# Kernel optimization log

Hardware: AMD Instinct MI355X
Metric: run time of the kernel (lower is better)

The kernel has to match this reference:

```python
import jax, jax.numpy as jnp
import numpy as np

# Circuit structure constants (HCLT-style tensorized probabilistic circuit)
V = 128      # num_vars
M = 256      # num_latents (input nodes per variable)
C = 64       # num categories per variable
B = 256      # batch size
L = 4        # number of inner (prod, sum) layer pairs
N = 32768    # sum nodes per inner layer
K = 4        # sum-node fanin (children product elements per sum node)
A = 2        # product-node arity
E = N * K    # product elements per layer
NUM_INPUT = V * M


def setup_inputs() -> dict:
    key = jax.random.key(0)
    k1, k2, k3, k4 = jax.random.split(key, 4)
    inputs = jax.random.randint(k1, (B, V), 0, C)                          # [B, V] categorical data
    input_logits = jax.random.normal(k2, (NUM_INPUT, C), dtype=jnp.float32)  # per input-node categorical logits
    sum_logits = jax.random.normal(k3, (L, N, K), dtype=jnp.float32)         # per sum-node edge logits (grouped softmax)
    root_logits = jax.random.normal(k4, (N,), dtype=jnp.float32)             # root sum-node edge logits
    # Irregular child index structure: prod element e in layer l gathers A children
    # from any node computed so far (dummy node 0 excluded, indices >= 1).
    rng = np.random.default_rng(0)
    base = 1 + NUM_INPUT
    child = np.stack([rng.integers(1, base + l * N, size=(E, A)) for l in range(L)], axis=0)
    prod_child_ids = jnp.asarray(child, dtype=jnp.int32)                    # [L, E, A]
    return {"inputs": inputs, "input_logits": input_logits, "sum_logits": sum_logits,
            "root_logits": root_logits, "prod_child_ids": prod_child_ids}


def reference(inputs, input_logits, sum_logits, root_logits, prod_child_ids):
    # --- input layer: node_mars for input nodes = log p(x_{vid(n)} | node n) ---
    logp = jax.nn.log_softmax(input_logits, axis=-1)            # [VM, C]
    vids = jnp.arange(NUM_INPUT) // M                           # variable id per input node
    cats = inputs[:, vids].T                                    # [VM, B] category index per (node, batch)
    in_mars = jnp.take_along_axis(logp, cats, axis=1)           # [VM, B]
    # node 0 is the dummy node with log-marginal 0.0 (as in the original buffer init)
    node_buf = jnp.concatenate([jnp.zeros((1, B), dtype=in_mars.dtype), in_mars], axis=0)
    # --- inner layers: alternating ProdLayer (gather+add) and SumLayer (softmax params + logsumexp) ---
    for l in range(L):
        ch = node_buf[prod_child_ids[l]]                        # [E, A, B] irregular gather
        elem = ch.sum(axis=1)                                   # element_mars: [E, B]
        logw = jax.nn.log_softmax(sum_logits[l], axis=-1)       # per-node grouped softmax: [N, K]
        nodes = jax.nn.logsumexp(elem.reshape(N, K, B) + logw[:, :, None], axis=1)  # [N, B]
        node_buf = jnp.concatenate([node_buf, nodes], axis=0)
    # --- root sum node ---
    rw = jax.nn.log_softmax(root_logits)                        # [N]
    lls = jax.nn.logsumexp(node_buf[-N:] + rw[:, None], axis=0) # [B]
    return lls[:, None]                                         # [B, num_roots=1]
```

## Files before the change

### kernel.cpp

```cpp
#include <hip/hip_runtime.h>
#include <math.h>

#define V 128
#define M 256
#define CAT 64
#define B 256
#define LAYERS 4
#define N 32768
#define K 4
#define AR 2
#define E (N * K)
#define NUM_INPUT (V * M)
#define BASE (1 + NUM_INPUT)
#define TOTAL_ROWS (BASE + LAYERS * N)
#define PPART 256

typedef _Float16 half8 __attribute__((ext_vector_type(8)));
typedef _Float16 half4 __attribute__((ext_vector_type(4)));
typedef float float8_t __attribute__((ext_vector_type(8)));

#define OFF_IN 5.2f
__device__ __forceinline__ float layer_off(int l) {
    const float o[4] = {11.4f, 23.5f, 47.5f, 95.5f};
    return o[l];
}
__device__ __forceinline__ float row_off(int row) {
    return (row < BASE) ? OFF_IN : layer_off((row - BASE) >> 15);
}

__global__ __launch_bounds__(256) void input_layer_kernel(
    const int* __restrict__ inputs,
    const float* __restrict__ input_logits,
    _Float16* __restrict__ buf)
{
    __shared__ float lg[4][CAT];
    __shared__ int cats[B];
    __shared__ float lzs[4];
    const int t = threadIdx.x;
    const int n0 = blockIdx.x * 4;

    lg[t >> 6][t & 63] = input_logits[(size_t)n0 * CAT + t];
    cats[t] = inputs[t * V + (n0 >> 8)];
    __syncthreads();

    const int w = t >> 6;
    const int l = t & 63;
    float x = lg[w][l];
    float m = x;
    #pragma unroll
    for (int off = 32; off >= 1; off >>= 1) m = fmaxf(m, __shfl_xor(m, off));
    float s = __expf(x - m);
    #pragma unroll
    for (int off = 32; off >= 1; off >>= 1) s += __shfl_xor(s, off);
    if (l == 0) lzs[w] = m + __logf(s);
    __syncthreads();

    const float logZ = lzs[w];
    half4 r;
    #pragma unroll
    for (int j = 0; j < 4; ++j) {
        const int c = cats[4 * l + j];
        r[j] = (_Float16)(lg[w][c] - logZ + OFF_IN);
    }
    ((half4*)buf)[(size_t)(1 + n0 + w) * (B / 4) + l] = r;

    if (blockIdx.x == 0 && t < B / 4) {
        half4 z;
        z[0] = z[1] = z[2] = z[3] = (_Float16)OFF_IN;
        ((half4*)buf)[t] = z;
    }
}

__global__ __launch_bounds__(256) void layer_kernel(
    const int* __restrict__ child,
    const float* __restrict__ slog,
    _Float16* __restrict__ buf,
    int out_row0, int layer)
{
    __shared__ int ch[8][K * AR];
    __shared__ float w[8][K];
    const int t = threadIdx.x;
    const int i0 = blockIdx.x * 8;

    if (t < 64) ((int*)ch)[t] = child[(size_t)i0 * (K * AR) + t];
    __syncthreads();

    if (t < 32) {
        const float x = slog[(size_t)i0 * K + t];
        float mm = fmaxf(x, __shfl_xor(x, 1));
        mm = fmaxf(mm, __shfl_xor(mm, 2));
        float e = __expf(x - mm);
        float ss = e + __shfl_xor(e, 1);
        ss += __shfl_xor(ss, 2);
        const float lz = mm + __logf(ss);
        const int j = t >> 2, k = t & 3;
        w[j][k] = x - lz - row_off(ch[j][2 * k]) - row_off(ch[j][2 * k + 1])
                  + layer_off(layer);
    }
    __syncthreads();

    const int g = t >> 5;
    const int l = t & 31;
    const half8* bufv = (const half8*)buf;

    float8_t v[K];
    #pragma unroll
    for (int k = 0; k < K; ++k) {
        const half8 a = bufv[ch[g][2 * k]     * (B / 8) + l];
        const half8 b = bufv[ch[g][2 * k + 1] * (B / 8) + l];
        v[k] = __builtin_convertvector(a, float8_t) +
               __builtin_convertvector(b, float8_t) + w[g][k];
    }

    half8 r;
    #pragma unroll
    for (int j = 0; j < 8; ++j) {
        const float mm = fmaxf(fmaxf(v[0][j], v[1][j]), fmaxf(v[2][j], v[3][j]));
        const float ss = __expf(v[0][j] - mm) + __expf(v[1][j] - mm) +
                         __expf(v[2][j] - mm) + __expf(v[3][j] - mm);
        r[j] = (_Float16)(mm + __logf(ss));
    }
    ((half8*)buf)[(out_row0 + i0 + g) * (B / 8) + l] = r;
}

__global__ __launch_bounds__(256) void root_partial_kernel(
    const _Float16* __restrict__ buf,
    const float* __restrict__ rlog,
    float* __restrict__ pm, float* __restrict__ ps)
{
    const int p = blockIdx.x;
    const int t = threadIdx.x;
    const _Float16* last = buf + (size_t)(BASE + (LAYERS - 1) * N) * B;
    const float off3 = layer_off(LAYERS - 1);

    float m0 = -INFINITY, s0 = 0.f, m1 = -INFINITY, s1 = 0.f;
    float m2 = -INFINITY, s2 = 0.f, m3 = -INFINITY, s3 = 0.f;

    #define ONL(mm, ss, vv) { const float nm = fmaxf(mm, vv); \
        ss = ss * __expf(mm - nm) + __expf(vv - nm); mm = nm; }

    for (int n = p; n < N; n += 4 * PPART) {
        const float v0 = (float)last[(size_t)(n)             * B + t] + (rlog[n]             - off3);
        const float v1 = (float)last[(size_t)(n + PPART)     * B + t] + (rlog[n + PPART]     - off3);
        const float v2 = (float)last[(size_t)(n + 2 * PPART) * B + t] + (rlog[n + 2 * PPART] - off3);
        const float v3 = (float)last[(size_t)(n + 3 * PPART) * B + t] + (rlog[n + 3 * PPART] - off3);
        ONL(m0, s0, v0);
        ONL(m1, s1, v1);
        ONL(m2, s2, v2);
        ONL(m3, s3, v3);
    }
    ONL(m0, s0, m1 + __logf(s1));
    ONL(m2, s2, m3 + __logf(s3));
    ONL(m0, s0, m2 + __logf(s2));
    #undef ONL

    pm[p * B + t] = m0;
    ps[p * B + t] = s0;
}

__global__ __launch_bounds__(256) void root_combine_kernel(
    const float* __restrict__ rlog,
    const float* __restrict__ pm, const float* __restrict__ ps,
    float* __restrict__ out)
{
    __shared__ float red[256];
    const int t = threadIdx.x;

    float a0 = -INFINITY, a1 = -INFINITY, a2 = -INFINITY, a3 = -INFINITY;
    #pragma unroll 4
    for (int n = t; n < N; n += 1024) {
        a0 = fmaxf(a0, rlog[n]);
        a1 = fmaxf(a1, rlog[n + 256]);
        a2 = fmaxf(a2, rlog[n + 512]);
        a3 = fmaxf(a3, rlog[n + 768]);
    }
    red[t] = fmaxf(fmaxf(a0, a1), fmaxf(a2, a3));
    __syncthreads();
    for (int off = 128; off >= 1; off >>= 1) {
        if (t < off) red[t] = fmaxf(red[t], red[t + off]);
        __syncthreads();
    }
    const float gm = red[0];
    __syncthreads();

    float b0 = 0.f, b1 = 0.f, b2 = 0.f, b3 = 0.f;
    #pragma unroll 4
    for (int n = t; n < N; n += 1024) {
        b0 += __expf(rlog[n]       - gm);
        b1 += __expf(rlog[n + 256] - gm);
        b2 += __expf(rlog[n + 512] - gm);
        b3 += __expf(rlog[n + 768] - gm);
    }
    red[t] = (b0 + b1) + (b2 + b3);
    __syncthreads();
    for (int off = 128; off >= 1; off >>= 1) {
        if (t < off) red[t] += red[t + off];
        __syncthreads();
    }
    const float logZ = gm + __logf(red[0]);

    float m0 = -INFINITY, m1 = -INFINITY, m2 = -INFINITY, m3 = -INFINITY;
    #pragma unroll 8
    for (int p = 0; p < PPART; p += 4) {
        m0 = fmaxf(m0, pm[(p)     * B + t]);
        m1 = fmaxf(m1, pm[(p + 1) * B + t]);
        m2 = fmaxf(m2, pm[(p + 2) * B + t]);
        m3 = fmaxf(m3, pm[(p + 3) * B + t]);
    }
    const float m = fmaxf(fmaxf(m0, m1), fmaxf(m2, m3));

    float s0 = 0.f, s1 = 0.f, s2 = 0.f, s3 = 0.f;
    #pragma unroll 8
    for (int p = 0; p < PPART; p += 4) {
        s0 += ps[(p)     * B + t] * __expf(pm[(p)     * B + t] - m);
        s1 += ps[(p + 1) * B + t] * __expf(pm[(p + 1) * B + t] - m);
        s2 += ps[(p + 2) * B + t] * __expf(pm[(p + 2) * B + t] - m);
        s3 += ps[(p + 3) * B + t] * __expf(pm[(p + 3) * B + t] - m);
    }
    out[t] = m + __logf((s0 + s1) + (s2 + s3)) - logZ;
}

extern "C" void kernel_launch(void* const* d_in, const int* in_sizes, int n_in,
                              void* d_out, int out_size, void* d_ws, size_t ws_size,
                              hipStream_t stream) {
    const int*   inputs       = (const int*)d_in[0];
    const float* input_logits = (const float*)d_in[1];
    const float* sum_logits   = (const float*)d_in[2];
    const float* root_logits  = (const float*)d_in[3];
    const int*   child        = (const int*)d_in[4];
    float* out = (float*)d_out;

    _Float16* buf = (_Float16*)d_ws;
    float* pm = (float*)(buf + (size_t)TOTAL_ROWS * B);
    float* ps = pm + (size_t)PPART * B;

    input_layer_kernel<<<NUM_INPUT / 4, 256, 0, stream>>>(inputs, input_logits, buf);

    for (int l = 0; l < LAYERS; ++l) {
        layer_kernel<<<N / 8, 256, 0, stream>>>(
            child + (size_t)l * E * AR,
            sum_logits + (size_t)l * N * K,
            buf,
            BASE + l * N, l);
    }

    root_partial_kernel<<<PPART, 256, 0, stream>>>(buf, root_logits, pm, ps);
    root_combine_kernel<<<1, 256, 0, stream>>>(root_logits, pm, ps, out);
}
```

Before: 143.7 us.

## Fuse last sum layer with root partial logsumexp reduction

The last inner layer is computed inside a new 1024-thread kernel that folds in the root weights and reduces each 32-node block to a per-batch (max, sum) partial in shared memory, so layer-3 outputs are never written to or re-read from global memory. A two-stage reduction (root_reduce1 then root_combine) merges the 1024 partials. This removes a 16 MB write plus re-read and a kernel launch, but adds a shared-memory transpose, an extra small kernel, and lower per-block parallelism during the reduction phase.

New measurement: 127.9 us. 1.12x faster.

```diff
diff --git a/kernel.cpp b/kernel.cpp
--- a/kernel.cpp
+++ b/kernel.cpp
@@ -13,7 +13,9 @@
 #define NUM_INPUT (V * M)
 #define BASE (1 + NUM_INPUT)
 #define TOTAL_ROWS (BASE + LAYERS * N)
-#define PPART 256
+#define L3N 32
+#define NPART (N / L3N)
+#define R1BLK 32
 
 typedef _Float16 half8 __attribute__((ext_vector_type(8)));
 typedef _Float16 half4 __attribute__((ext_vector_type(4)));
@@ -123,44 +125,97 @@
     ((half8*)buf)[(out_row0 + i0 + g) * (B / 8) + l] = r;
 }
 
-__global__ __launch_bounds__(256) void root_partial_kernel(
+__global__ __launch_bounds__(1024) void layer3_root_kernel(
+    const int* __restrict__ child,
+    const float* __restrict__ slog,
     const _Float16* __restrict__ buf,
     const float* __restrict__ rlog,
     float* __restrict__ pm, float* __restrict__ ps)
 {
-    const int p = blockIdx.x;
+    __shared__ int ch[L3N][K * AR];
+    __shared__ float w[L3N][K];
+    __shared__ float rl[L3N];
+    __shared__ float vmat[B][L3N + 1];
     const int t = threadIdx.x;
-    const _Float16* last = buf + (size_t)(BASE + (LAYERS - 1) * N) * B;
-    const float off3 = layer_off(LAYERS - 1);
-
-    float m0 = -INFINITY, s0 = 0.f, m1 = -INFINITY, s1 = 0.f;
-    float m2 = -INFINITY, s2 = 0.f, m3 = -INFINITY, s3 = 0.f;
-
-    #define ONL(mm, ss, vv) { const float nm = fmaxf(mm, vv); \
-        ss = ss * __expf(mm - nm) + __expf(vv - nm); mm = nm; }
-
-    for (int n = p; n < N; n += 4 * PPART) {
-        const float v0 = (float)last[(size_t)(n)             * B + t] + (rlog[n]             - off3);
-        const float v1 = (float)last[(size_t)(n + PPART)     * B + t] + (rlog[n + PPART]     - off3);
-        const float v2 = (float)last[(size_t)(n + 2 * PPART) * B + t] + (rlog[n + 2 * PPART] - off3);
-        const float v3 = (float)last[(size_t)(n + 3 * PPART) * B + t] + (rlog[n + 3 * PPART] - off3);
-        ONL(m0, s0, v0);
-        ONL(m1, s1, v1);
-        ONL(m2, s2, v2);
-        ONL(m3, s3, v3);
-    }
-    ONL(m0, s0, m1 + __logf(s1));
-    ONL(m2, s2, m3 + __logf(s3));
-    ONL(m0, s0, m2 + __logf(s2));
-    #undef ONL
-
-    pm[p * B + t] = m0;
-    ps[p * B + t] = s0;
+    const int i0 = blockIdx.x * L3N;
+    const float off3 = layer_off(3);
+
+    if (t < L3N * 8) ((int*)ch)[t] = child[(size_t)i0 * (K * AR) + t];
+    if (t >= 512 && t < 512 + L3N) rl[t - 512] = rlog[i0 + (t - 512)];
+    __syncthreads();
+
+    if (t < L3N * 4) {
+        const float x = slog[(size_t)i0 * K + t];
+        float mm = fmaxf(x, __shfl_xor(x, 1));
+        mm = fmaxf(mm, __shfl_xor(mm, 2));
+        float e = __expf(x - mm);
+        float ss = e + __shfl_xor(e, 1);
+        ss += __shfl_xor(ss, 2);
+        const float lz = mm + __logf(ss);
+        const int j = t >> 2, k = t & 3;
+        w[j][k] = x - lz - row_off(ch[j][2 * k]) - row_off(ch[j][2 * k + 1])
+                  + off3;
+    }
+    __syncthreads();
+
+    const int g = t >> 5;
+    const int l = t & 31;
+
+    const half8* bufv = (const half8*)buf;
+    float8_t v[K];
+    #pragma unroll
+    for (int k = 0; k < K; ++k) {
+        const half8 a = bufv[ch[g][2 * k]     * (B / 8) + l];
+        const half8 b = bufv[ch[g][2 * k + 1] * (B / 8) + l];
+        v[k] = __builtin_convertvector(a, float8_t) +
+               __builtin_convertvector(b, float8_t) + w[g][k];
+    }
+
+    const float radd = rl[g] - off3;
+    #pragma unroll
+    for (int j = 0; j < 8; ++j) {
+        const float mm = fmaxf(fmaxf(v[0][j], v[1][j]), fmaxf(v[2][j], v[3][j]));
+        const float ss = __expf(v[0][j] - mm) + __expf(v[1][j] - mm) +
+                         __expf(v[2][j] - mm) + __expf(v[3][j] - mm);
+        vmat[8 * l + j][g] = mm + __logf(ss) + radd;
+    }
+    __syncthreads();
+
+    if (t < B) {
+        float m = -INFINITY;
+        #pragma unroll
+        for (int q = 0; q < L3N; ++q) m = fmaxf(m, vmat[t][q]);
+        float s = 0.0f;
+        #pragma unroll
+        for (int q = 0; q < L3N; ++q) s += __expf(vmat[t][q] - m);
+        pm[blockIdx.x * B + t] = m;
+        ps[blockIdx.x * B + t] = s;
+    }
+}
+
+__global__ __launch_bounds__(256) void root_reduce1(
+    const float* __restrict__ pm, const float* __restrict__ ps,
+    float* __restrict__ pm2, float* __restrict__ ps2)
+{
+    const int j = blockIdx.x;
+    const int c = threadIdx.x;
+    const int Q = NPART / R1BLK;
+    const int p0 = j * Q;
+
+    float m = -INFINITY;
+    #pragma unroll 8
+    for (int q = 0; q < Q; ++q) m = fmaxf(m, pm[(p0 + q) * B + c]);
+    float s = 0.0f;
+    #pragma unroll 8
+    for (int q = 0; q < Q; ++q)
+        s += ps[(p0 + q) * B + c] * __expf(pm[(p0 + q) * B + c] - m);
+    pm2[j * B + c] = m;
+    ps2[j * B + c] = s;
 }
 
 __global__ __launch_bounds__(256) void root_combine_kernel(
     const float* __restrict__ rlog,
-    const float* __restrict__ pm, const float* __restrict__ ps,
+    const float* __restrict__ pm2, const float* __restrict__ ps2,
     float* __restrict__ out)
 {
     __shared__ float red[256];
@@ -199,25 +254,14 @@
     }
     const float logZ = gm + __logf(red[0]);
 
-    float m0 = -INFINITY, m1 = -INFINITY, m2 = -INFINITY, m3 = -INFINITY;
+    float m = -INFINITY;
     #pragma unroll 8
-    for (int p = 0; p < PPART; p += 4) {
-        m0 = fmaxf(m0, pm[(p)     * B + t]);
-        m1 = fmaxf(m1, pm[(p + 1) * B + t]);
-        m2 = fmaxf(m2, pm[(p + 2) * B + t]);
-        m3 = fmaxf(m3, pm[(p + 3) * B + t]);
-    }
-    const float m = fmaxf(fmaxf(m0, m1), fmaxf(m2, m3));
-
-    float s0 = 0.f, s1 = 0.f, s2 = 0.f, s3 = 0.f;
+    for (int p = 0; p < R1BLK; ++p) m = fmaxf(m, pm2[p * B + t]);
+    float s = 0.0f;
     #pragma unroll 8
-    for (int p = 0; p < PPART; p += 4) {
-        s0 += ps[(p)     * B + t] * __expf(pm[(p)     * B + t] - m);
-        s1 += ps[(p + 1) * B + t] * __expf(pm[(p + 1) * B + t] - m);
-        s2 += ps[(p + 2) * B + t] * __expf(pm[(p + 2) * B + t] - m);
-        s3 += ps[(p + 3) * B + t] * __expf(pm[(p + 3) * B + t] - m);
-    }
-    out[t] = m + __logf((s0 + s1) + (s2 + s3)) - logZ;
+    for (int p = 0; p < R1BLK; ++p)
+        s += ps2[p * B + t] * __expf(pm2[p * B + t] - m);
+    out[t] = m + __logf(s) - logZ;
 }
 
 extern "C" void kernel_launch(void* const* d_in, const int* in_sizes, int n_in,
@@ -231,12 +275,14 @@
     float* out = (float*)d_out;
 
     _Float16* buf = (_Float16*)d_ws;
-    float* pm = (float*)(buf + (size_t)TOTAL_ROWS * B);
-    float* ps = pm + (size_t)PPART * B;
+    float* pm  = (float*)(buf + (size_t)TOTAL_ROWS * B);
+    float* ps  = pm  + (size_t)NPART * B;
+    float* pm2 = ps  + (size_t)NPART * B;
+    float* ps2 = pm2 + (size_t)R1BLK * B;
 
     input_layer_kernel<<<NUM_INPUT / 4, 256, 0, stream>>>(inputs, input_logits, buf);
 
-    for (int l = 0; l < LAYERS; ++l) {
+    for (int l = 0; l < LAYERS - 1; ++l) {
         layer_kernel<<<N / 8, 256, 0, stream>>>(
             child + (size_t)l * E * AR,
             sum_logits + (size_t)l * N * K,
@@ -244,6 +290,11 @@
             BASE + l * N, l);
     }
 
-    root_partial_kernel<<<PPART, 256, 0, stream>>>(buf, root_logits, pm, ps);
-    root_combine_kernel<<<1, 256, 0, stream>>>(root_logits, pm, ps, out);
-}
+    layer3_root_kernel<<<NPART, 1024, 0, stream>>>(
+        child + (size_t)(LAYERS - 1) * E * AR,
+        sum_logits + (size_t)(LAYERS - 1) * N * K,
+        buf, root_logits, pm, ps);
+
+    root_reduce1<<<R1BLK, 256, 0, stream>>>(pm, ps, pm2, ps2);
+    root_combine_kernel<<<1, 256, 0, stream>>>(root_logits, pm2, ps2, out);
+}
```

## Fuse last layer with root partial reduction and batch more nodes per block

Applied to the files above, without the earlier changes.

The last inner layer is fused with the root partial logsumexp, so the final 32768x256 half buffer is never written and re-read. Inside the fused kernel, per-node results are transposed through shared memory and reduced per batch column. The input layer now handles 16 nodes per block and gathers categories with lane shuffles instead of shared memory. The inner layer kernel handles 16 nodes per block and issues all 16 gathers before computing. The fused kernel runs only 256 blocks of 1024 threads with several barriers per iteration, which may limit parallelism.

New measurement: 131.4 us. -8.5%, faster.

```diff
diff --git a/kernel.cpp b/kernel.cpp
--- a/kernel.cpp
+++ b/kernel.cpp
@@ -6,14 +6,16 @@
 #define CAT 64
 #define B 256
 #define LAYERS 4
-#define N 32768
 #define K 4
 #define AR 2
-#define E (N * K)
+#define NNODES 32768
+#define E (NNODES * K)
 #define NUM_INPUT (V * M)
 #define BASE (1 + NUM_INPUT)
-#define TOTAL_ROWS (BASE + LAYERS * N)
-#define PPART 256
+#define TOTAL_ROWS (BASE + LAYERS * NNODES)
+#define L3BLKS 256
+#define L3ITER 4
+#define NPART 256
 
 typedef _Float16 half8 __attribute__((ext_vector_type(8)));
 typedef _Float16 half4 __attribute__((ext_vector_type(4)));
@@ -21,11 +23,11 @@
 
 #define OFF_IN 5.2f
 __device__ __forceinline__ float layer_off(int l) {
-    const float o[4] = {11.4f, 23.5f, 47.5f, 95.5f};
-    return o[l];
+    return (l == 0) ? 11.4f : (l == 1) ? 23.5f : (l == 2) ? 47.5f : 95.5f;
 }
 __device__ __forceinline__ float row_off(int row) {
-    return (row < BASE) ? OFF_IN : layer_off((row - BASE) >> 15);
+    if (row < BASE) return OFF_IN;
+    return layer_off((row - BASE) >> 15);
 }
 
 __global__ __launch_bounds__(256) void input_layer_kernel(
@@ -33,36 +35,39 @@
     const float* __restrict__ input_logits,
     _Float16* __restrict__ buf)
 {
-    __shared__ float lg[4][CAT];
     __shared__ int cats[B];
-    __shared__ float lzs[4];
     const int t = threadIdx.x;
-    const int n0 = blockIdx.x * 4;
-
-    lg[t >> 6][t & 63] = input_logits[(size_t)n0 * CAT + t];
-    cats[t] = inputs[t * V + (n0 >> 8)];
-    __syncthreads();
-
+    const int n0 = blockIdx.x * 16;
+    const int vid = n0 >> 8;
+
+    cats[t] = inputs[t * V + vid];
+    __syncthreads();
+
+    const int l = t & 63;
     const int w = t >> 6;
-    const int l = t & 63;
-    float x = lg[w][l];
-    float m = x;
-    #pragma unroll
-    for (int off = 32; off >= 1; off >>= 1) m = fmaxf(m, __shfl_xor(m, off));
-    float s = __expf(x - m);
-    #pragma unroll
-    for (int off = 32; off >= 1; off >>= 1) s += __shfl_xor(s, off);
-    if (l == 0) lzs[w] = m + __logf(s);
-    __syncthreads();
-
-    const float logZ = lzs[w];
-    half4 r;
-    #pragma unroll
-    for (int j = 0; j < 4; ++j) {
-        const int c = cats[4 * l + j];
-        r[j] = (_Float16)(lg[w][c] - logZ + OFF_IN);
-    }
-    ((half4*)buf)[(size_t)(1 + n0 + w) * (B / 4) + l] = r;
+    const int c0 = cats[4 * l + 0];
+    const int c1 = cats[4 * l + 1];
+    const int c2 = cats[4 * l + 2];
+    const int c3 = cats[4 * l + 3];
+
+    #pragma unroll
+    for (int it = 0; it < 4; ++it) {
+        const int n = n0 + it * 4 + w;
+        const float x = input_logits[n * CAT + l];
+        float m = x;
+        #pragma unroll
+        for (int off = 32; off >= 1; off >>= 1) m = fmaxf(m, __shfl_xor(m, off));
+        float s = __expf(x - m);
+        #pragma unroll
+        for (int off = 32; off >= 1; off >>= 1) s += __shfl_xor(s, off);
+        const float logZ = m + __logf(s);
+        half4 r;
+        r[0] = (_Float16)(__shfl(x, c0) - logZ + OFF_IN);
+        r[1] = (_Float16)(__shfl(x, c1) - logZ + OFF_IN);
+        r[2] = (_Float16)(__shfl(x, c2) - logZ + OFF_IN);
+        r[3] = (_Float16)(__shfl(x, c3) - logZ + OFF_IN);
+        ((half4*)buf)[(1 + n) * (B / 4) + l] = r;
+    }
 
     if (blockIdx.x == 0 && t < B / 4) {
         half4 z;
@@ -77,15 +82,15 @@
     _Float16* __restrict__ buf,
     int out_row0, int layer)
 {
-    __shared__ int ch[8][K * AR];
-    __shared__ float w[8][K];
+    __shared__ int ch[16][K * AR];
+    __shared__ float w[16][K];
     const int t = threadIdx.x;
-    const int i0 = blockIdx.x * 8;
-
-    if (t < 64) ((int*)ch)[t] = child[(size_t)i0 * (K * AR) + t];
-    __syncthreads();
-
-    if (t < 32) {
+    const int i0 = blockIdx.x * 16;
+
+    if (t < 128) ((int*)ch)[t] = child[(size_t)i0 * (K * AR) + t];
+    __syncthreads();
+
+    if (t < 64) {
         const float x = slog[(size_t)i0 * K + t];
         float mm = fmaxf(x, __shfl_xor(x, 1));
         mm = fmaxf(mm, __shfl_xor(mm, 2));
@@ -100,65 +105,122 @@
     __syncthreads();
 
     const int g = t >> 5;
-    const int l = t & 31;
+    const int lane = t & 31;
     const half8* bufv = (const half8*)buf;
 
-    float8_t v[K];
-    #pragma unroll
-    for (int k = 0; k < K; ++k) {
-        const half8 a = bufv[ch[g][2 * k]     * (B / 8) + l];
-        const half8 b = bufv[ch[g][2 * k + 1] * (B / 8) + l];
-        v[k] = __builtin_convertvector(a, float8_t) +
-               __builtin_convertvector(b, float8_t) + w[g][k];
-    }
-
-    half8 r;
+    half8 ra[8], rb[8];
+    #pragma unroll
+    for (int c = 0; c < 8; ++c) ra[c] = bufv[ch[g][c]     * (B / 8) + lane];
+    #pragma unroll
+    for (int c = 0; c < 8; ++c) rb[c] = bufv[ch[8 + g][c] * (B / 8) + lane];
+
+    float8_t va[K];
+    #pragma unroll
+    for (int k = 0; k < K; ++k)
+        va[k] = __builtin_convertvector(ra[2 * k], float8_t) +
+                __builtin_convertvector(ra[2 * k + 1], float8_t) + w[g][k];
+    half8 rA;
     #pragma unroll
     for (int j = 0; j < 8; ++j) {
-        const float mm = fmaxf(fmaxf(v[0][j], v[1][j]), fmaxf(v[2][j], v[3][j]));
-        const float ss = __expf(v[0][j] - mm) + __expf(v[1][j] - mm) +
-                         __expf(v[2][j] - mm) + __expf(v[3][j] - mm);
-        r[j] = (_Float16)(mm + __logf(ss));
-    }
-    ((half8*)buf)[(out_row0 + i0 + g) * (B / 8) + l] = r;
-}
-
-__global__ __launch_bounds__(256) void root_partial_kernel(
+        const float mm = fmaxf(fmaxf(va[0][j], va[1][j]), fmaxf(va[2][j], va[3][j]));
+        const float ss = __expf(va[0][j] - mm) + __expf(va[1][j] - mm) +
+                         __expf(va[2][j] - mm) + __expf(va[3][j] - mm);
+        rA[j] = (_Float16)(mm + __logf(ss));
+    }
+    ((half8*)buf)[(out_row0 + i0 + g) * (B / 8) + lane] = rA;
+
+    float8_t vb[K];
+    #pragma unroll
+    for (int k = 0; k < K; ++k)
+        vb[k] = __builtin_convertvector(rb[2 * k], float8_t) +
+                __builtin_convertvector(rb[2 * k + 1], float8_t) + w[8 + g][k];
+    half8 rB;
+    #pragma unroll
+    for (int j = 0; j < 8; ++j) {
+        const float mm = fmaxf(fmaxf(vb[0][j], vb[1][j]), fmaxf(vb[2][j], vb[3][j]));
+        const float ss = __expf(vb[0][j] - mm) + __expf(vb[1][j] - mm) +
+                         __expf(vb[2][j] - mm) + __expf(vb[3][j] - mm);
+        rB[j] = (_Float16)(mm + __logf(ss));
+    }
+    ((half8*)buf)[(out_row0 + i0 + 8 + g) * (B / 8) + lane] = rB;
+}
+
+__global__ __launch_bounds__(1024) void layer3_root_kernel(
+    const int* __restrict__ child,
+    const float* __restrict__ slog,
     const _Float16* __restrict__ buf,
     const float* __restrict__ rlog,
     float* __restrict__ pm, float* __restrict__ ps)
 {
-    const int p = blockIdx.x;
+    __shared__ int ch[32][K * AR];
+    __shared__ float w[32][K];
+    __shared__ float rl[32];
+    __shared__ float vmat[B][33];
     const int t = threadIdx.x;
-    const _Float16* last = buf + (size_t)(BASE + (LAYERS - 1) * N) * B;
-    const float off3 = layer_off(LAYERS - 1);
-
-    float m0 = -INFINITY, s0 = 0.f, m1 = -INFINITY, s1 = 0.f;
-    float m2 = -INFINITY, s2 = 0.f, m3 = -INFINITY, s3 = 0.f;
-
-    #define ONL(mm, ss, vv) { const float nm = fmaxf(mm, vv); \
-        ss = ss * __expf(mm - nm) + __expf(vv - nm); mm = nm; }
-
-    for (int n = p; n < N; n += 4 * PPART) {
-        const float v0 = (float)last[(size_t)(n)             * B + t] + (rlog[n]             - off3);
-        const float v1 = (float)last[(size_t)(n + PPART)     * B + t] + (rlog[n + PPART]     - off3);
-        const float v2 = (float)last[(size_t)(n + 2 * PPART) * B + t] + (rlog[n + 2 * PPART] - off3);
-        const float v3 = (float)last[(size_t)(n + 3 * PPART) * B + t] + (rlog[n + 3 * PPART] - off3);
-        ONL(m0, s0, v0);
-        ONL(m1, s1, v1);
-        ONL(m2, s2, v2);
-        ONL(m3, s3, v3);
-    }
-    ONL(m0, s0, m1 + __logf(s1));
-    ONL(m2, s2, m3 + __logf(s3));
-    ONL(m0, s0, m2 + __logf(s2));
-    #undef ONL
-
-    pm[p * B + t] = m0;
-    ps[p * B + t] = s0;
-}
-
-__global__ __launch_bounds__(256) void root_combine_kernel(
+    const float off3 = layer_off(3);
+    const int g = t >> 5;
+    const int lane = t & 31;
+
+    float mB = -INFINITY, sB = 0.0f;
+
+    for (int it = 0; it < L3ITER; ++it) {
+        const int i0 = (blockIdx.x * L3ITER + it) * 32;
+        __syncthreads();
+        if (t < 256) ((int*)ch)[t] = child[(size_t)i0 * (K * AR) + t];
+        if (t >= 512 && t < 544) rl[t - 512] = rlog[i0 + (t - 512)];
+        __syncthreads();
+        if (t < 128) {
+            const float x = slog[(size_t)i0 * K + t];
+            float mm = fmaxf(x, __shfl_xor(x, 1));
+            mm = fmaxf(mm, __shfl_xor(mm, 2));
+            float e = __expf(x - mm);
+            float ss = e + __shfl_xor(e, 1);
+            ss += __shfl_xor(ss, 2);
+            const float lz = mm + __logf(ss);
+            const int j = t >> 2, k = t & 3;
+            w[j][k] = x - lz - row_off(ch[j][2 * k]) - row_off(ch[j][2 * k + 1])
+                      + off3;
+        }
+        __syncthreads();
+
+        const half8* bufv = (const half8*)buf;
+        float8_t v[K];
+        #pragma unroll
+        for (int k = 0; k < K; ++k) {
+            const half8 a = bufv[ch[g][2 * k]     * (B / 8) + lane];
+            const half8 b = bufv[ch[g][2 * k + 1] * (B / 8) + lane];
+            v[k] = __builtin_convertvector(a, float8_t) +
+                   __builtin_convertvector(b, float8_t) + w[g][k];
+        }
+        const float radd = rl[g] - off3;
+        #pragma unroll
+        for (int j = 0; j < 8; ++j) {
+            const float mm = fmaxf(fmaxf(v[0][j], v[1][j]), fmaxf(v[2][j], v[3][j]));
+            const float ss = __expf(v[0][j] - mm) + __expf(v[1][j] - mm) +
+                             __expf(v[2][j] - mm) + __expf(v[3][j] - mm);
+            vmat[8 * lane + j][g] = mm + __logf(ss) + radd;
+        }
+        __syncthreads();
+
+        if (t < B) {
+            float m8 = vmat[t][0];
+            #pragma unroll
+            for (int q = 1; q < 32; ++q) m8 = fmaxf(m8, vmat[t][q]);
+            float s8 = 0.0f;
+            #pragma unroll
+            for (int q = 0; q < 32; ++q) s8 += __expf(vmat[t][q] - m8);
+            const float nm = fmaxf(mB, m8);
+            sB = sB * __expf(mB - nm) + s8 * __expf(m8 - nm);
+            mB = nm;
+        }
+    }
+    if (t < B) {
+        pm[blockIdx.x * B + t] = mB;
+        ps[blockIdx.x * B + t] = sB;
+    }
+}
+
+__global__ __launch_bounds__(256) void root_final_kernel(
     const float* __restrict__ rlog,
     const float* __restrict__ pm, const float* __restrict__ ps,
     float* __restrict__ out)
@@ -168,7 +230,7 @@
 
     float a0 = -INFINITY, a1 = -INFINITY, a2 = -INFINITY, a3 = -INFINITY;
     #pragma unroll 4
-    for (int n = t; n < N; n += 1024) {
+    for (int n = t; n < NNODES; n += 1024) {
         a0 = fmaxf(a0, rlog[n]);
         a1 = fmaxf(a1, rlog[n + 256]);
         a2 = fmaxf(a2, rlog[n + 512]);
@@ -185,7 +247,7 @@
 
     float b0 = 0.f, b1 = 0.f, b2 = 0.f, b3 = 0.f;
     #pragma unroll 4
-    for (int n = t; n < N; n += 1024) {
+    for (int n = t; n < NNODES; n += 1024) {
         b0 += __expf(rlog[n]       - gm);
         b1 += __expf(rlog[n + 256] - gm);
         b2 += __expf(rlog[n + 512] - gm);
@@ -201,7 +263,7 @@
 
     float m0 = -INFINITY, m1 = -INFINITY, m2 = -INFINITY, m3 = -INFINITY;
     #pragma unroll 8
-    for (int p = 0; p < PPART; p += 4) {
+    for (int p = 0; p < NPART; p += 4) {
         m0 = fmaxf(m0, pm[(p)     * B + t]);
         m1 = fmaxf(m1, pm[(p + 1) * B + t]);
         m2 = fmaxf(m2, pm[(p + 2) * B + t]);
@@ -211,7 +273,7 @@
 
     float s0 = 0.f, s1 = 0.f, s2 = 0.f, s3 = 0.f;
     #pragma unroll 8
-    for (int p = 0; p < PPART; p += 4) {
+    for (int p = 0; p < NPART; p += 4) {
         s0 += ps[(p)     * B + t] * __expf(pm[(p)     * B + t] - m);
         s1 += ps[(p + 1) * B + t] * __expf(pm[(p + 1) * B + t] - m);
         s2 += ps[(p + 2) * B + t] * __expf(pm[(p + 2) * B + t] - m);
@@ -232,18 +294,21 @@
 
     _Float16* buf = (_Float16*)d_ws;
     float* pm = (float*)(buf + (size_t)TOTAL_ROWS * B);
-    float* ps = pm + (size_t)PPART * B;
-
-    input_layer_kernel<<<NUM_INPUT / 4, 256, 0, stream>>>(inputs, input_logits, buf);
-
-    for (int l = 0; l < LAYERS; ++l) {
-        layer_kernel<<<N / 8, 256, 0, stream>>>(
+    float* ps = pm + (size_t)NPART * B;
+
+    input_layer_kernel<<<NUM_INPUT / 16, 256, 0, stream>>>(inputs, input_logits, buf);
+
+    for (int l = 0; l < LAYERS - 1; ++l) {
+        layer_kernel<<<NNODES / 16, 256, 0, stream>>>(
             child + (size_t)l * E * AR,
-            sum_logits + (size_t)l * N * K,
-            buf,
-            BASE + l * N, l);
-    }
-
-    root_partial_kernel<<<PPART, 256, 0, stream>>>(buf, root_logits, pm, ps);
-    root_combine_kernel<<<1, 256, 0, stream>>>(root_logits, pm, ps, out);
-}
+            sum_logits + (size_t)l * NNODES * K,
+            buf, BASE + l * NNODES, l);
+    }
+
+    layer3_root_kernel<<<L3BLKS, 1024, 0, stream>>>(
+        child + (size_t)(LAYERS - 1) * E * AR,
+        sum_logits + (size_t)(LAYERS - 1) * NNODES * K,
+        buf, root_logits, pm, ps);
+
+    root_final_kernel<<<1, 256, 0, stream>>>(root_logits, pm, ps, out);
+}
```
